# Kernel tuning notes

Hardware: AMD Instinct MI355X
Metric: run time of the kernel (lower is better)

## Reference

```python
import jax, jax.numpy as jnp
import numpy as np

B, T, F, H = 8, 1024, 256, 256
EPS = 1e-5


def layer_norm(x, w, b):
    m = jnp.mean(x, axis=-1, keepdims=True)
    v = jnp.var(x, axis=-1, keepdims=True)
    return (x - m) / jnp.sqrt(v + EPS) * w + b


def setup_inputs() -> dict:
    key = jax.random.key(0)
    ks = jax.random.split(key, 8)
    x = jax.random.normal(ks[0], (B, T, F, 2), dtype=jnp.float32)
    # 8 attention branches, each with its own q/k/v Linear(F -> H).
    # Stored as [8, F, H] (already transposed vs torch's [out,in]).
    Wq = jax.random.normal(ks[1], (8, F, H), dtype=jnp.float32) * 0.02
    Wk = jax.random.normal(ks[2], (8, F, H), dtype=jnp.float32) * 0.02
    Wv = jax.random.normal(ks[3], (8, F, H), dtype=jnp.float32) * 0.02
    bq = jax.random.normal(ks[4], (8, H), dtype=jnp.float32) * 0.02
    bk = jax.random.normal(ks[5], (8, H), dtype=jnp.float32) * 0.02
    bv = jax.random.normal(ks[6], (8, H), dtype=jnp.float32) * 0.02
    ln1_w = jnp.ones((F,), jnp.float32)
    ln1_b = jnp.zeros((F,), jnp.float32)
    ln2_w = jnp.ones((H,), jnp.float32)
    ln2_b = jnp.zeros((H,), jnp.float32)
    return {"x": x, "Wq": Wq, "bq": bq, "Wk": Wk, "bk": bk, "Wv": Wv,
            "bv": bv, "ln1_w": ln1_w, "ln1_b": ln1_b,
            "ln2_w": ln2_w, "ln2_b": ln2_b}


def reference(x, Wq, bq, Wk, bk, Wv, bv, ln1_w, ln1_b, ln2_w, ln2_b):
    # LayerNorm over the in_channel (frequency) axis, per real/imag plane
    xn = jnp.swapaxes(layer_norm(jnp.swapaxes(x, 2, 3), ln1_w, ln1_b), 2, 3)
    real, imag = xn[..., 0], xn[..., 1]  # each [B,T,F]
    # branch order: A(r,r,r) B(r,i,i) C(i,r,i) D(i,i,r) E(r,r,i) F(r,i,r) G(i,r,r) H(i,i,i)
    qs = jnp.stack([real, real, imag, imag, real, real, imag, imag])  # [8,B,T,F]
    ks_ = jnp.stack([real, imag, real, imag, real, imag, real, imag])
    vs = jnp.stack([real, imag, imag, real, imag, real, real, imag])
    q = jnp.einsum('nbtf,nfh->nbth', qs, Wq) + bq[:, None, None, :]
    k = jnp.einsum('nbtf,nfh->nbth', ks_, Wk) + bk[:, None, None, :]
    v = jnp.einsum('nbtf,nfh->nbth', vs, Wv) + bv[:, None, None, :]
    scale = 1.0 / (Wq.shape[-1] ** 0.5)
    energy = jnp.einsum('nbth,nbsh->nbts', q, k) * scale  # [8,B,T,T]
    attn = jax.nn.softmax(energy, axis=-1)
    o = jnp.einsum('nbts,nbsh->nbth', attn, v)  # [8,B,T,H]
    real_att = o[0] - o[1] - o[2] - o[3]
    imag_att = o[4] + o[5] + o[6] - o[7]
    out = jnp.stack([real_att, imag_att], axis=-1)  # [B,T,H,2]
    out = jnp.swapaxes(layer_norm(jnp.swapaxes(out, 2, 3), ln2_w, ln2_b), 2, 3)
    return out
```

## Files before the change

kernel.cpp:

```cpp
#include <hip/hip_runtime.h>
#include <math.h>

#define B_ 8
#define T_ 1024
#define F_ 256
#define H_ 256
#define BT_ (B_*T_)
constexpr float EPS = 1e-5f;
constexpr float SCALE = 0.0625f;

typedef unsigned int u32;
typedef unsigned short u16;
typedef __attribute__((ext_vector_type(8))) short bf16x8;
typedef __attribute__((ext_vector_type(4))) float f32x4;
typedef __attribute__((ext_vector_type(16))) float f32x16;

__device__ __forceinline__ float bflo(u32 p) { return __uint_as_float(p << 16); }
__device__ __forceinline__ float bfhi(u32 p) { return __uint_as_float(p & 0xFFFF0000u); }
__device__ __forceinline__ float bf1(u16 p) { return __uint_as_float(((u32)p) << 16); }
__device__ __forceinline__ u16 f2bf(float f) {
  u32 u = __float_as_uint(f);
  u32 r = u + 0x7FFFu + ((u >> 16) & 1u);
  return (u16)(r >> 16);
}

__device__ __forceinline__ f32x4 mfma16(bf16x8 a, bf16x8 b, f32x4 c) {
  return __builtin_amdgcn_mfma_f32_16x16x32_bf16(a, b, c, 0, 0, 0);
}
__device__ __forceinline__ f32x16 mfma32(bf16x8 a, bf16x8 b, f32x16 c) {
  return __builtin_amdgcn_mfma_f32_32x32x16_bf16(a, b, c, 0, 0, 0);
}

__device__ __forceinline__ void gload_lds16(const u16* g, u16* l) {
  __builtin_amdgcn_global_load_lds(
      (const __attribute__((address_space(1))) u32*)(uintptr_t)g,
      (__attribute__((address_space(3))) u32*)(u32)(uintptr_t)l,
      16, 0, 0);
}

__device__ __forceinline__ void block_reduce4(float& a, float& b, float& c, float& d) {
  #pragma unroll
  for (int off = 32; off > 0; off >>= 1) {
    a += __shfl_down(a, off, 64);
    b += __shfl_down(b, off, 64);
    c += __shfl_down(c, off, 64);
    d += __shfl_down(d, off, 64);
  }
  __shared__ float red[4][4];
  int wid = threadIdx.x >> 6;
  int lane = threadIdx.x & 63;
  if (lane == 0) { red[0][wid] = a; red[1][wid] = b; red[2][wid] = c; red[3][wid] = d; }
  __syncthreads();
  a = red[0][0] + red[0][1] + red[0][2] + red[0][3];
  b = red[1][0] + red[1][1] + red[1][2] + red[1][3];
  c = red[2][0] + red[2][1] + red[2][2] + red[2][3];
  d = red[3][0] + red[3][1] + red[3][2] + red[3][3];
}

__global__ __launch_bounds__(256) void ln1_kernel(
    const float* __restrict__ x, const float* __restrict__ w, const float* __restrict__ bi,
    u16* __restrict__ xnr, u16* __restrict__ xni) {
  const int row = blockIdx.x;
  const int f = threadIdx.x;
  float2 xv = reinterpret_cast<const float2*>(x)[row * F_ + f];
  float sr = xv.x, si = xv.y, sr2 = xv.x * xv.x, si2 = xv.y * xv.y;
  block_reduce4(sr, si, sr2, si2);
  const float inv = 1.0f / F_;
  float mr = sr * inv, mi = si * inv;
  float vr = sr2 * inv - mr * mr, vi = si2 * inv - mi * mi;
  float rr = rsqrtf(vr + EPS), ri = rsqrtf(vi + EPS);
  float ww = w[f], bb = bi[f];
  xnr[row * F_ + f] = f2bf((xv.x - mr) * rr * ww + bb);
  xni[row * F_ + f] = f2bf((xv.y - mi) * ri * ww + bb);
}

__global__ __launch_bounds__(256) void wprep_kernel(
    const float* __restrict__ Wq, const float* __restrict__ Wk, const float* __restrict__ Wv,
    u16* __restrict__ wT) {
  const int z = blockIdx.z;
  const int m = z >> 3, n = z & 7;
  const float* W = (m == 0 ? Wq : (m == 1 ? Wk : Wv)) + (size_t)n * F_ * H_;
  const int ft = blockIdx.x * 64;
  const int ht = blockIdx.y * 64;
  __shared__ __align__(16) u16 Ts[64][72];

  const int tid = threadIdx.x;
  #pragma unroll
  for (int i = 0; i < 4; i++) {
    int id = tid + i * 256;
    int r = id >> 4, c4 = (id & 15) * 4;
    float4 p = *reinterpret_cast<const float4*>(&W[(size_t)(ft + r) * H_ + ht + c4]);
    Ts[r][c4 + 0] = f2bf(p.x); Ts[r][c4 + 1] = f2bf(p.y);
    Ts[r][c4 + 2] = f2bf(p.z); Ts[r][c4 + 3] = f2bf(p.w);
  }
  __syncthreads();
  u16* op = wT + (size_t)z * F_ * H_ + (size_t)ht * F_ + ft;
  #pragma unroll
  for (int i = 0; i < 2; i++) {
    int id = tid + i * 256;
    int hl = id & 63, g = id >> 6;
    u16 tmp[8];
    #pragma unroll
    for (int j = 0; j < 8; j++) tmp[j] = Ts[g * 8 + j][hl];
    *reinterpret_cast<uint4*>(op + (size_t)hl * F_ + g * 8) =
        *reinterpret_cast<const uint4*>(tmp);
  }
}

__global__ __launch_bounds__(256, 2) void qkv_kernel(
    const u16* __restrict__ xnr, const u16* __restrict__ xni, const u16* __restrict__ wT,
    const float* __restrict__ bq, const float* __restrict__ bk, const float* __restrict__ bv,
    u16* __restrict__ qo, u16* __restrict__ ko, u16* __restrict__ vTo) {
  const int z = blockIdx.y;
  const int m = z >> 3, n = z & 7;
  int sel; const float* bias; u16* out;
  if (m == 0)      { sel = (n >> 1) & 1;  bias = bq; out = qo + (size_t)n * BT_ * H_; }
  else if (m == 1) { sel = n & 1;         bias = bk; out = ko + (size_t)n * BT_ * H_; }
  else             { sel = __popc(n) & 1; bias = bv; out = nullptr; }
  const float osc = (m == 0) ? SCALE : 1.0f;
  const u16* A = sel ? xni : xnr;
  const u16* wp = wT + (size_t)z * F_ * H_;
  bias += n * H_;
  const int rowbase = blockIdx.x * 128;

  __shared__ __align__(16) u16 As[2][128 * 32];
  __shared__ __align__(16) u16 Bs[2][256 * 32];
  __shared__ __align__(16) u16 Epi[4][1536];

  const int tid = threadIdx.x;
  const int wv = tid >> 6, lane = tid & 63;
  const int quad = lane >> 4, l16 = lane & 15;
  const int wrow = wv >> 1, wcol = wv & 1;

  f32x4 acc[4][8];
  #pragma unroll
  for (int i = 0; i < 4; i++)
    #pragma unroll
    for (int j = 0; j < 8; j++) acc[i][j] = (f32x4){0.f, 0.f, 0.f, 0.f};

  const int ar = tid >> 2;
  const int ak = (tid & 3) * 8;

  #pragma unroll 1
  for (int kb = 0; kb < F_; kb += 64) {
    #pragma unroll
    for (int h = 0; h < 2; h++) {
      gload_lds16(A + (size_t)(rowbase + ar) * F_ + kb + h * 32 + ak,
                  &As[h][tid * 8]);
      gload_lds16(A + (size_t)(rowbase + 64 + ar) * F_ + kb + h * 32 + ak,
                  &As[h][2048 + tid * 8]);
      #pragma unroll
      for (int c = 0; c < 4; c++)
        gload_lds16(wp + (size_t)(c * 64 + ar) * F_ + kb + h * 32 + ak,
                    &Bs[h][c * 2048 + tid * 8]);
    }
    __syncthreads();
    #pragma unroll
    for (int h = 0; h < 2; h++) {
      bf16x8 a[4], b[8];
      #pragma unroll
      for (int mi = 0; mi < 4; mi++)
        a[mi] = *reinterpret_cast<const bf16x8*>(
            &As[h][(wrow * 64 + mi * 16 + l16) * 32 + quad * 8]);
      #pragma unroll
      for (int nj = 0; nj < 8; nj++)
        b[nj] = *reinterpret_cast<const bf16x8*>(
            &Bs[h][(wcol * 128 + nj * 16 + l16) * 32 + quad * 8]);
      #pragma unroll
      for (int mi = 0; mi < 4; mi++)
        #pragma unroll
        for (int nj = 0; nj < 8; nj++)
          acc[mi][nj] = mfma16(a[mi], b[nj], acc[mi][nj]);
    }
    __syncthreads();
  }

  float bias8[8];
  #pragma unroll
  for (int nj = 0; nj < 8; nj++)
    bias8[nj] = bias[wcol * 128 + nj * 16 + l16];

  if (m != 2) {
    #pragma unroll
    for (int pass = 0; pass < 2; pass++) {
      #pragma unroll
      for (int mi = 0; mi < 4; mi++) {
        #pragma unroll
        for (int nj4 = 0; nj4 < 4; nj4++) {
          int nj = pass * 4 + nj4;
          #pragma unroll
          for (int r = 0; r < 4; r++)
            Epi[wv][(quad * 4 + r) * 72 + nj4 * 16 + l16] =
                f2bf((acc[mi][nj][r] + bias8[nj]) * osc);
        }
        int row = rowbase + wrow * 64 + mi * 16 + l16;
        uint4 v0 = *reinterpret_cast<const uint4*>(&Epi[wv][l16 * 72 + quad * 16]);
        uint4 v1 = *reinterpret_cast<const uint4*>(&Epi[wv][l16 * 72 + quad * 16 + 8]);
        u16* op = out + (size_t)row * H_ + wcol * 128 + pass * 64 + quad * 16;
        *reinterpret_cast<uint4*>(op) = v0;
        *reinterpret_cast<uint4*>(op + 8) = v1;
      }
    }
  } else {
    #pragma unroll
    for (int pass = 0; pass < 2; pass++) {
      #pragma unroll
      for (int mi = 0; mi < 4; mi++) {
        #pragma unroll
        for (int nj4 = 0; nj4 < 4; nj4++) {
          int nj = pass * 4 + nj4;
          #pragma unroll
          for (int r = 0; r < 4; r++)
            Epi[wv][(nj4 * 16 + l16) * 24 + quad * 4 + r] =
                f2bf(acc[mi][nj][r] + bias8[nj]);
        }
        int hloc = lane;
        uint4 w0 = *reinterpret_cast<const uint4*>(&Epi[wv][hloc * 24]);
        uint4 w1 = *reinterpret_cast<const uint4*>(&Epi[wv][hloc * 24 + 8]);
        u16* op = vTo + (size_t)n * H_ * BT_ +
                  (size_t)(wcol * 128 + pass * 64 + hloc) * BT_ +
                  rowbase + wrow * 64 + mi * 16;
        *reinterpret_cast<uint4*>(op) = w0;
        *reinterpret_cast<uint4*>(op + 8) = w1;
      }
    }
  }
}

__global__ __launch_bounds__(256, 2) void attn_kernel(
    const u16* __restrict__ q, const u16* __restrict__ k, const u16* __restrict__ vT,
    u16* __restrict__ obuf) {
  const int qt = blockIdx.x;
  const int nb = blockIdx.y;
  const int n = nb >> 3, b = nb & 7;
  const int tid = threadIdx.x;
  const int wv = tid >> 6, lane = tid & 63;
  const int hi = lane >> 5, l32 = lane & 31;
  const int qh = wv >> 1;
  const int kh = wv & 1;
  const int hh = wv & 1;

  const size_t base = (size_t)nb * T_ * H_;
  const u16* qp = q + base;
  const u16* kp = k + base;
  const u16* vtp = vT + ((size_t)n * H_ * B_ + b) * T_;

  __shared__ __align__(16) u16 Ks[64][264];
  __shared__ __align__(16) u16 Vs[256][72];
  __shared__ __align__(16) u16 Ps[2][32][72];

  const int qrow0 = qt * 64 + qh * 32;
  bf16x8 qf[16];
  #pragma unroll
  for (int kc = 0; kc < 16; kc++)
    qf[kc] = *reinterpret_cast<const bf16x8*>(
        qp + (size_t)(qrow0 + l32) * H_ + kc * 16 + hi * 8);

  f32x16 o[4];
  #pragma unroll
  for (int ot = 0; ot < 4; ot++)
    #pragma unroll
    for (int r = 0; r < 16; r++) o[ot][r] = 0.f;
  float lper[16];
  #pragma unroll
  for (int r = 0; r < 16; r++) lper[r] = 0.f;

  const int krow = tid >> 2, kch = tid & 3;
  const int vrow4 = tid >> 2, vkc = tid & 3;

  #pragma unroll 1
  for (int kt = 0; kt < 16; kt++) {
    __syncthreads();
    {
      uint4 kreg[8], vreg[4][2];
      #pragma unroll
      for (int i = 0; i < 8; i++)
        kreg[i] = *reinterpret_cast<const uint4*>(
            kp + (size_t)(kt * 64 + krow) * H_ + kch * 8 + i * 32);
      #pragma unroll
      for (int p = 0; p < 4; p++) {
        vreg[p][0] = *reinterpret_cast<const uint4*>(
            vtp + (size_t)(p * 64 + vrow4) * BT_ + kt * 64 + vkc * 16);
        vreg[p][1] = *reinterpret_cast<const uint4*>(
            vtp + (size_t)(p * 64 + vrow4) * BT_ + kt * 64 + vkc * 16 + 8);
      }
      #pragma unroll
      for (int i = 0; i < 8; i++)
        *reinterpret_cast<uint4*>(&Ks[krow][kch * 8 + i * 32]) = kreg[i];
      #pragma unroll
      for (int p = 0; p < 4; p++) {
        *reinterpret_cast<uint4*>(&Vs[p * 64 + vrow4][vkc * 16]) = vreg[p][0];
        *reinterpret_cast<uint4*>(&Vs[p * 64 + vrow4][vkc * 16 + 8]) = vreg[p][1];
      }
    }
    __syncthreads();

    f32x16 sa, sb;
    #pragma unroll
    for (int r = 0; r < 16; r++) { sa[r] = 0.f; sb[r] = 0.f; }
    #pragma unroll
    for (int kc = 0; kc < 16; kc += 2) {
      bf16x8 kfa = *reinterpret_cast<const bf16x8*>(
          &Ks[kh * 32 + l32][kc * 16 + hi * 8]);
      bf16x8 kfb = *reinterpret_cast<const bf16x8*>(
          &Ks[kh * 32 + l32][(kc + 1) * 16 + hi * 8]);
      sa = mfma32(qf[kc], kfa, sa);
      sb = mfma32(qf[kc + 1], kfb, sb);
    }
    #pragma unroll
    for (int r = 0; r < 16; r++) {
      float p = __expf(sa[r] + sb[r]);
      lper[r] += p;
      Ps[qh][(r & 3) + 8 * (r >> 2) + 4 * hi][kh * 32 + l32] = f2bf(p);
    }
    __syncthreads();

    bf16x8 pa[4];
    #pragma unroll
    for (int kc2 = 0; kc2 < 4; kc2++)
      pa[kc2] = *reinterpret_cast<const bf16x8*>(
          &Ps[qh][l32][kc2 * 16 + hi * 8]);
    #pragma unroll
    for (int ot = 0; ot < 4; ot++)
      #pragma unroll
      for (int kc2 = 0; kc2 < 4; kc2++) {
        bf16x8 vf = *reinterpret_cast<const bf16x8*>(
            &Vs[hh * 128 + ot * 32 + l32][kc2 * 16 + hi * 8]);
        o[ot] = mfma32(pa[kc2], vf, o[ot]);
      }
  }

  #pragma unroll
  for (int r = 0; r < 16; r++) {
    #pragma unroll
    for (int off = 1; off < 32; off <<= 1)
      lper[r] += __shfl_xor(lper[r], off, 64);
  }
  if (l32 == 0) {
    #pragma unroll
    for (int r = 0; r < 16; r++) {
      int row = (r & 3) + 8 * (r >> 2) + 4 * hi;
      *reinterpret_cast<float*>(&Ps[qh][row][64 + 2 * kh]) = lper[r];
    }
  }
  __syncthreads();

  float invl[16];
  #pragma unroll
  for (int r = 0; r < 16; r++) {
    int row = (r & 3) + 8 * (r >> 2) + 4 * hi;
    float l0 = *reinterpret_cast<const float*>(&Ps[qh][row][64]);
    float l1 = *reinterpret_cast<const float*>(&Ps[qh][row][66]);
    invl[r] = 1.0f / (l0 + l1);
  }

  u16* Ew = reinterpret_cast<u16*>(&Ks[0][0]) + wv * 1280;
  const int grow = b * 1024 + qrow0 + l32;
  #pragma unroll
  for (int ot = 0; ot < 4; ot++) {
    #pragma unroll
    for (int r = 0; r < 16; r++) {
      int row = (r & 3) + 8 * (r >> 2) + 4 * hi;
      Ew[row * 40 + l32] = f2bf(o[ot][r] * invl[r]);
    }
    int ht = hh * 4 + ot;
    uint4 v0 = *reinterpret_cast<const uint4*>(&Ew[l32 * 40 + hi * 16]);
    uint4 v1 = *reinterpret_cast<const uint4*>(&Ew[l32 * 40 + hi * 16 + 8]);
    u16* op = obuf + (((size_t)n * 8 + ht) * BT_ + grow) * 32 + hi * 16;
    *reinterpret_cast<uint4*>(op) = v0;
    *reinterpret_cast<uint4*>(op + 8) = v1;
  }
}

__global__ __launch_bounds__(256) void combine_ln2_kernel(
    const u16* __restrict__ obuf, const float* __restrict__ w,
    const float* __restrict__ bi, float* __restrict__ out) {
  const int row = blockIdx.x;
  const int h = threadIdx.x;
  float o[8];
  #pragma unroll
  for (int nn = 0; nn < 8; nn++)
    o[nn] = bf1(obuf[(((size_t)nn * 8 + (h >> 5)) * BT_ + row) * 32 + (h & 31)]);
  float re = o[0] - o[1] - o[2] - o[3];
  float im = o[4] + o[5] + o[6] - o[7];
  float sr = re, si = im, sr2 = re * re, si2 = im * im;
  block_reduce4(sr, si, sr2, si2);
  const float inv = 1.0f / H_;
  float mr = sr * inv, mi = si * inv;
  float vr = sr2 * inv - mr * mr, vi = si2 * inv - mi * mi;
  float rr = rsqrtf(vr + EPS), ri = rsqrtf(vi + EPS);
  float ww = w[h], bb = bi[h];
  float2 res;
  res.x = (re - mr) * rr * ww + bb;
  res.y = (im - mi) * ri * ww + bb;
  reinterpret_cast<float2*>(out)[(size_t)row * H_ + h] = res;
}

extern "C" void kernel_launch(void* const* d_in, const int* in_sizes, int n_in,
                              void* d_out, int out_size, void* d_ws, size_t ws_size,
                              hipStream_t stream) {
  const float* x    = (const float*)d_in[0];
  const float* Wq   = (const float*)d_in[1];
  const float* bq   = (const float*)d_in[2];
  const float* Wk   = (const float*)d_in[3];
  const float* bk   = (const float*)d_in[4];
  const float* Wv   = (const float*)d_in[5];
  const float* bv   = (const float*)d_in[6];
  const float* ln1w = (const float*)d_in[7];
  const float* ln1b = (const float*)d_in[8];
  const float* ln2w = (const float*)d_in[9];
  const float* ln2b = (const float*)d_in[10];

  char* ws = (char*)d_ws;
  u16* xnr  = (u16*)(ws);
  u16* xni  = (u16*)(ws + (4ull  << 20));
  u16* wTb  = (u16*)(ws + (8ull  << 20));
  u16* obuf = (u16*)(ws);
  u16* vT   = (u16*)(ws + (32ull << 20));
  u16* qbuf = (u16*)(ws + (64ull << 20));
  u16* kbuf = (u16*)(ws + (96ull << 20));

  ln1_kernel<<<BT_, 256, 0, stream>>>(x, ln1w, ln1b, xnr, xni);
  wprep_kernel<<<dim3(4, 4, 24), 256, 0, stream>>>(Wq, Wk, Wv, wTb);
  qkv_kernel<<<dim3(64, 24), 256, 0, stream>>>(xnr, xni, wTb, bq, bk, bv,
                                               qbuf, kbuf, vT);
  attn_kernel<<<dim3(16, 64), 256, 0, stream>>>(qbuf, kbuf, vT, obuf);
  combine_ln2_kernel<<<BT_, 256, 0, stream>>>(obuf, ln2w, ln2b, (float*)d_out);
}
```

Baseline: 190.2 us.

## Double-buffer K via direct global-to-LDS loads and read V straight into registers

```diff
diff --git a/kernel.cpp b/kernel.cpp
--- a/kernel.cpp
+++ b/kernel.cpp
@@ -245,8 +245,7 @@
   const u16* kp = k + base;
   const u16* vtp = vT + ((size_t)n * H_ * B_ + b) * T_;
 
-  __shared__ __align__(16) u16 Ks[64][264];
-  __shared__ __align__(16) u16 Vs[256][72];
+  __shared__ __align__(16) u16 Ks[2][64][256];
   __shared__ __align__(16) u16 Ps[2][32][72];
 
   const int qrow0 = qt * 64 + qh * 32;
@@ -265,48 +264,60 @@
   #pragma unroll
   for (int r = 0; r < 16; r++) lper[r] = 0.f;
 
-  const int krow = tid >> 2, kch = tid & 3;
-  const int vrow4 = tid >> 2, vkc = tid & 3;
-
+  auto stage_k = [&](int ktN, int buf) {
+    #pragma unroll
+    for (int i = 0; i < 8; i++) {
+      int idx = wv * 8 + i;
+      int row = 2 * idx + hi;
+      const u16* src = kp + (size_t)(ktN * 64 + row) * H_ +
+                       ((l32 * 8) ^ ((row & 7) * 8));
+      gload_lds16(src, &Ks[buf][2 * idx][0]);
+    }
+  };
+
+  stage_k(0, 0);
+  __syncthreads();
+
+  const int krow = kh * 32 + l32;
+  const int ksw = (krow & 7) * 8;
+
+  int cur = 0;
   #pragma unroll 1
   for (int kt = 0; kt < 16; kt++) {
-    __syncthreads();
-    {
-      uint4 kreg[8], vreg[4][2];
-      #pragma unroll
-      for (int i = 0; i < 8; i++)
-        kreg[i] = *reinterpret_cast<const uint4*>(
-            kp + (size_t)(kt * 64 + krow) * H_ + kch * 8 + i * 32);
-      #pragma unroll
-      for (int p = 0; p < 4; p++) {
-        vreg[p][0] = *reinterpret_cast<const uint4*>(
-            vtp + (size_t)(p * 64 + vrow4) * BT_ + kt * 64 + vkc * 16);
-        vreg[p][1] = *reinterpret_cast<const uint4*>(
-            vtp + (size_t)(p * 64 + vrow4) * BT_ + kt * 64 + vkc * 16 + 8);
-      }
-      #pragma unroll
-      for (int i = 0; i < 8; i++)
-        *reinterpret_cast<uint4*>(&Ks[krow][kch * 8 + i * 32]) = kreg[i];
-      #pragma unroll
-      for (int p = 0; p < 4; p++) {
-        *reinterpret_cast<uint4*>(&Vs[p * 64 + vrow4][vkc * 16]) = vreg[p][0];
-        *reinterpret_cast<uint4*>(&Vs[p * 64 + vrow4][vkc * 16 + 8]) = vreg[p][1];
-      }
-    }
-    __syncthreads();
+    if (kt < 15) stage_k(kt + 1, cur ^ 1);
+
+    bf16x8 vreg[4][4];
+    #pragma unroll
+    for (int ot = 0; ot < 2; ot++)
+      #pragma unroll
+      for (int kc2 = 0; kc2 < 4; kc2++)
+        vreg[ot][kc2] = *reinterpret_cast<const bf16x8*>(
+            vtp + (size_t)(hh * 128 + ot * 32 + l32) * BT_ +
+            kt * 64 + kc2 * 16 + hi * 8);
 
     f32x16 sa, sb;
     #pragma unroll
     for (int r = 0; r < 16; r++) { sa[r] = 0.f; sb[r] = 0.f; }
+    __builtin_amdgcn_s_setprio(1);
     #pragma unroll
     for (int kc = 0; kc < 16; kc += 2) {
       bf16x8 kfa = *reinterpret_cast<const bf16x8*>(
-          &Ks[kh * 32 + l32][kc * 16 + hi * 8]);
+          &Ks[cur][krow][(kc * 16 + hi * 8) ^ ksw]);
       bf16x8 kfb = *reinterpret_cast<const bf16x8*>(
-          &Ks[kh * 32 + l32][(kc + 1) * 16 + hi * 8]);
+          &Ks[cur][krow][((kc + 1) * 16 + hi * 8) ^ ksw]);
       sa = mfma32(qf[kc], kfa, sa);
       sb = mfma32(qf[kc + 1], kfb, sb);
     }
+    __builtin_amdgcn_s_setprio(0);
+
+    #pragma unroll
+    for (int ot = 2; ot < 4; ot++)
+      #pragma unroll
+      for (int kc2 = 0; kc2 < 4; kc2++)
+        vreg[ot][kc2] = *reinterpret_cast<const bf16x8*>(
+            vtp + (size_t)(hh * 128 + ot * 32 + l32) * BT_ +
+            kt * 64 + kc2 * 16 + hi * 8);
+
     #pragma unroll
     for (int r = 0; r < 16; r++) {
       float p = __expf(sa[r] + sb[r]);
@@ -320,14 +331,15 @@
     for (int kc2 = 0; kc2 < 4; kc2++)
       pa[kc2] = *reinterpret_cast<const bf16x8*>(
           &Ps[qh][l32][kc2 * 16 + hi * 8]);
+    __builtin_amdgcn_s_setprio(1);
     #pragma unroll
     for (int ot = 0; ot < 4; ot++)
       #pragma unroll
-      for (int kc2 = 0; kc2 < 4; kc2++) {
-        bf16x8 vf = *reinterpret_cast<const bf16x8*>(
-            &Vs[hh * 128 + ot * 32 + l32][kc2 * 16 + hi * 8]);
-        o[ot] = mfma32(pa[kc2], vf, o[ot]);
-      }
+      for (int kc2 = 0; kc2 < 4; kc2++)
+        o[ot] = mfma32(pa[kc2], vreg[ot][kc2], o[ot]);
+    __builtin_amdgcn_s_setprio(0);
+    __syncthreads();
+    cur ^= 1;
   }
 
   #pragma unroll
@@ -354,7 +366,7 @@
     invl[r] = 1.0f / (l0 + l1);
   }
 
-  u16* Ew = reinterpret_cast<u16*>(&Ks[0][0]) + wv * 1280;
+  u16* Ew = reinterpret_cast<u16*>(&Ks[0][0][0]) + wv * 1280;
   const int grow = b * 1024 + qrow0 + l32;
   #pragma unroll
   for (int ot = 0; ot < 4; ot++) {
```

New measurement: 400.8 us. +110.7%, slower.
